# Kernel optimization log

Hardware: AMD Instinct MI355X
Metric: run time of the kernel (lower is better)

The kernel has to match this reference:

```python
import jax, jax.numpy as jnp
import numpy as np

V, E, H, T, B, L = 50000, 256, 256, 20, 64, 512
START, STOP = 18, 19
NEG = -10000.0


def setup_inputs() -> dict:
    key = jax.random.key(0)
    ks = jax.random.split(key, 16)
    lengths = jnp.sort(jax.random.randint(ks[0], (B,), 1, L + 1))[::-1]
    lengths = lengths.at[0].set(L)  # pack_padded requires sorted descending
    sentences = jax.random.randint(ks[1], (B, L), 0, V)
    s = lambda k, shp, sc: jax.random.normal(k, shp, jnp.float32) * sc
    trans = jax.random.normal(ks[12], (T, T), jnp.float32)
    trans = trans.at[START, :].set(NEG).at[:, STOP].set(NEG)
    return {
        "sentences": sentences,
        "lengths": lengths,
        "emb": s(ks[2], (V, E), 1.0),
        "w_ih_f": s(ks[3], (4 * H, E), 0.05),
        "w_hh_f": s(ks[4], (4 * H, H), 0.05),
        "b_ih_f": s(ks[5], (4 * H,), 0.05),
        "b_hh_f": s(ks[6], (4 * H,), 0.05),
        "w_ih_b": s(ks[7], (4 * H, E), 0.05),
        "w_hh_b": s(ks[8], (4 * H, H), 0.05),
        "b_ih_b": s(ks[9], (4 * H,), 0.05),
        "b_hh_b": s(ks[10], (4 * H,), 0.05),
        "w_out": s(ks[11], (T, 2 * H), 0.05),
        "b_out": s(ks[13], (T,), 0.05),
        "transitions": trans,
    }


def _lstm(x, mask, w_ih, w_hh, b_ih, b_hh):
    # x: [B,L,E]; mask: [B,L] bool. Masked scan == packed-sequence LSTM
    # (hidden frozen past length, outputs zero past length like pad_packed).
    h0 = jnp.zeros((x.shape[0], H), x.dtype)
    bias = b_ih + b_hh

    def step(carry, inp):
        h, c = carry
        xt, mt = inp
        g = xt @ w_ih.T + h @ w_hh.T + bias
        i, f, gg, o = jnp.split(g, 4, axis=-1)  # torch gate order i,f,g,o
        c_new = jax.nn.sigmoid(f) * c + jax.nn.sigmoid(i) * jnp.tanh(gg)
        h_new = jax.nn.sigmoid(o) * jnp.tanh(c_new)
        m = mt[:, None]
        h = jnp.where(m, h_new, h)
        c = jnp.where(m, c_new, c)
        return (h, c), jnp.where(m, h_new, 0.0)

    _, hs = jax.lax.scan(step, (h0, h0), (x.transpose(1, 0, 2), mask.T))
    return hs.transpose(1, 0, 2)  # [B,L,H]


def _emissions(sentences, lengths, emb, w_ih_f, w_hh_f, b_ih_f, b_hh_f,
               w_ih_b, w_hh_b, b_ih_b, b_hh_b, w_out, b_out):
    mask = jnp.arange(L)[None, :] < lengths[:, None]  # [B,L]
    embeds = emb[sentences]  # [B,L,E]
    out_f = _lstm(embeds, mask, w_ih_f, w_hh_f, b_ih_f, b_hh_f)
    # backward dir: reverse each sequence within its own length
    rev_idx = jnp.clip(lengths[:, None] - 1 - jnp.arange(L)[None, :], 0, L - 1)
    x_rev = jnp.take_along_axis(embeds, rev_idx[:, :, None], axis=1)
    h_rev = _lstm(x_rev, mask, w_ih_b, w_hh_b, b_ih_b, b_hh_b)
    out_b = jnp.take_along_axis(h_rev, rev_idx[:, :, None], axis=1) * mask[..., None]
    lstm_out = jnp.concatenate([out_f, out_b], axis=-1)  # [B,L,2H]
    return lstm_out @ w_out.T + b_out  # [B,L,T]


def _viterbi(scores, lengths, transitions):
    mask = jnp.arange(L)[None, :] < lengths[:, None]
    fv0 = jnp.full((B, T), NEG, scores.dtype).at[:, START].set(0.0)

    def step(fv, inp):
        sc_t, m_t = inp  # [B,T], [B]
        ntv = fv[:, None, :] + transitions[None]  # [B,T(next),T(prev)]
        best = jnp.argmax(ntv, axis=-1)
        fv_new = jnp.max(ntv, axis=-1) + sc_t
        fv = jnp.where(m_t[:, None], fv_new, fv)
        bp = jnp.where(m_t[:, None], best, STOP)
        return fv, bp

    fv, bps = jax.lax.scan(step, fv0, (scores.transpose(1, 0, 2), mask.T))
    terminal = fv + transitions[STOP][None, :]  # [B,T]
    last_best = jnp.argmax(terminal, axis=-1)  # [B]
    path_scores = jnp.take_along_axis(terminal, last_best[:, None], axis=1)[:, 0]

    # backtrace: j runs L-1..1; writes tag for position j-1 when j < length
    barange = jnp.arange(B)

    def back(cur, j):
        valid = j < lengths
        new = jnp.where(valid, bps[j, barange, cur], cur)
        return new, new

    js = jnp.arange(L - 1, 0, -1)
    _, tags_rev = jax.lax.scan(back, last_best, js)  # [L-1,B]
    tags = tags_rev[::-1].T  # [B,L-1], positions 0..L-2
    pos = jnp.arange(L)[None, :]
    paths = jnp.where(pos < (lengths - 1)[:, None],
                      jnp.pad(tags, ((0, 0), (0, 1))), 0)
    paths = paths.at[barange, lengths - 1].set(last_best)  # pad past length with 0
    return path_scores, paths


def reference(sentences, lengths, emb, w_ih_f, w_hh_f, b_ih_f, b_hh_f,
              w_ih_b, w_hh_b, b_ih_b, b_hh_b, w_out, b_out, transitions):
    scores = _emissions(sentences, lengths, emb, w_ih_f, w_hh_f, b_ih_f, b_hh_f,
                        w_ih_b, w_hh_b, b_ih_b, b_hh_b, w_out, b_out)
    path_scores, paths = _viterbi(scores, lengths, transitions)
    return path_scores, paths
```

## Files before the change

kernel.cpp:

```cpp
#include <hip/hip_runtime.h>
#include <hip/hip_bf16.h>
#include <math.h>

#define NV 50000
#define NE 256
#define NH 256
#define NT 20
#define NB 64
#define NL 512
#define TAG_START 18
#define TAG_STOP 19
#define NEGV -10000.0f

typedef unsigned short ushortT;
typedef __attribute__((ext_vector_type(4))) float f32x4;
typedef __attribute__((ext_vector_type(8))) short short8;

#define PINV(x) asm volatile("" : "+v"(x))

__device__ __forceinline__ float sigf_slow(float x) { return 1.0f / (1.0f + expf(-x)); }
__device__ __forceinline__ float fsig(float x) { return 1.0f / (1.0f + __expf(-x)); }
__device__ __forceinline__ float ftanh(float x) { return 1.0f - 2.0f / (1.0f + __expf(2.0f * x)); }
__device__ __forceinline__ ushortT f2bf(float f) {
    unsigned int u = __float_as_uint(f);
    u += 0x7fffu + ((u >> 16) & 1u);
    return (ushortT)(u >> 16);
}
__device__ __forceinline__ float bf2f(unsigned int bits16) {
    return __uint_as_float(bits16 << 16);
}


__global__ __launch_bounds__(256) void k_cvtw(
    const float* __restrict__ whh_f, const float* __restrict__ whh_b,
    const float* __restrict__ wih_f, const float* __restrict__ wih_b,
    ushortT* __restrict__ whh16, ushortT* __restrict__ wih16)
{
    int idx = blockIdx.x * 256 + threadIdx.x;
    const float* s; ushortT* d;
    switch (blockIdx.y) {
        case 0: s = whh_f; d = whh16;            break;
        case 1: s = whh_b; d = whh16 + 262144;   break;
        case 2: s = wih_f; d = wih16;            break;
        default: s = wih_b; d = wih16 + 262144;  break;
    }
    d[idx] = f2bf(s[idx]);
}

__global__ __launch_bounds__(1024) void k_bias(
    const float* __restrict__ bih_f, const float* __restrict__ bhh_f,
    const float* __restrict__ bih_b, const float* __restrict__ bhh_b,
    float* __restrict__ biasc)
{
    int n = threadIdx.x;
    if (blockIdx.x == 0) biasc[n] = bih_f[n] + bhh_f[n];
    else                 biasc[1024 + n] = bih_b[n] + bhh_b[n];
}

__global__
__attribute__((amdgpu_flat_work_group_size(512, 512)))
__attribute__((amdgpu_waves_per_eu(2, 2)))
void k_gin_mfma(
    const int* __restrict__ sent, const int* __restrict__ lens,
    const float* __restrict__ emb, const ushortT* __restrict__ wih16,
    const float* __restrict__ biasc, float* __restrict__ gin,
    int chunk_start, int CH)
{
    const int g = blockIdx.x, tsub = blockIdx.y;
    const int dir = blockIdx.z >> 1, half = blockIdx.z & 1;
    const int gmax = lens[g * 16];
    const int tt0 = tsub * 16;
    if (chunk_start + tt0 >= gmax) return;

    const int tid = threadIdx.x;
    const int w = tid >> 6, l = tid & 63, lr = l & 15, lg = l >> 4;

    __shared__ char x_raw[16 * 512];

    const int ucol = half * 128 + w * 16 + lr;
    short8 bfr[4][8];
    float bias_l[4];
    const ushortT* wsrc = wih16 + dir * 262144;
#pragma unroll
    for (int nt = 0; nt < 4; ++nt) {
        int col = nt * 256 + ucol;
        bias_l[nt] = biasc[dir * 1024 + col];
#pragma unroll
        for (int kt = 0; kt < 8; ++kt)
            bfr[nt][kt] = *(const short8*)(wsrc + (size_t)col * 256 + kt * 32 + lg * 8);
    }
#pragma unroll
    for (int nt = 0; nt < 4; ++nt) {
        PINV(bias_l[nt]);
#pragma unroll
        for (int kt = 0; kt < 8; ++kt) PINV(bfr[nt][kt]);
    }

    const int srow = tid >> 5, sseg = tid & 31;
    const int slen = lens[g * 16 + srow];
    const int sb = (g * 16 + srow) * 512;

    for (int i = 0; i < 16; ++i) {
        int tg = chunk_start + tt0 + i;
        if (tg >= gmax) break;

        int tsrc = dir ? (slen - 1 - tg) : tg;
        if (tsrc < 0) tsrc = 0;
        if (tsrc > 511) tsrc = 511;
        int tok = sent[sb + tsrc];
        const float* es = emb + (size_t)tok * 256 + sseg * 8;
        float4 e0 = *(const float4*)es;
        float4 e1 = *(const float4*)(es + 4);
        short8 xv;
        xv[0] = (short)f2bf(e0.x); xv[1] = (short)f2bf(e0.y);
        xv[2] = (short)f2bf(e0.z); xv[3] = (short)f2bf(e0.w);
        xv[4] = (short)f2bf(e1.x); xv[5] = (short)f2bf(e1.y);
        xv[6] = (short)f2bf(e1.z); xv[7] = (short)f2bf(e1.w);
        int sa = (srow * 512 + sseg * 16) ^ ((srow & 7) << 4);
        *(short8*)&x_raw[sa] = xv;
        __syncthreads();

        short8 af[8];
#pragma unroll
        for (int kt = 0; kt < 8; ++kt) {
            int a = (lr * 512 + kt * 64 + lg * 16) ^ ((lr & 7) << 4);
            af[kt] = *(const short8*)&x_raw[a];
        }
        f32x4 acc[4];
#pragma unroll
        for (int nt = 0; nt < 4; ++nt) {
            acc[nt][0] = bias_l[nt]; acc[nt][1] = bias_l[nt];
            acc[nt][2] = bias_l[nt]; acc[nt][3] = bias_l[nt];
        }
#pragma unroll
        for (int kt = 0; kt < 8; ++kt)
#pragma unroll
            for (int nt = 0; nt < 4; ++nt)
                acc[nt] = __builtin_amdgcn_mfma_f32_16x16x32_bf16(af[kt], bfr[nt][kt], acc[nt], 0, 0, 0);

        float* ginp = gin + ((size_t)((dir * 4 + g) * CH + (tt0 + i))) * 16384;
#pragma unroll
        for (int nt = 0; nt < 4; ++nt)
            *(f32x4*)(ginp + (nt * 256 + ucol) * 16 + lg * 4) = acc[nt];
        __syncthreads();
    }
}

__global__
__attribute__((amdgpu_flat_work_group_size(512, 512)))
__attribute__((amdgpu_waves_per_eu(2, 2)))
void k_rec_mfma(
    const int* __restrict__ lens, const ushortT* __restrict__ whh16,
    const float* __restrict__ gin, ushortT* __restrict__ hout,
    ushortT* __restrict__ st_h, float* __restrict__ st_c,
    ushortT* __restrict__ hex, unsigned int* __restrict__ flags,
    int chunk_start, int CH)
{
    const int g = blockIdx.x, dir = blockIdx.y, half = blockIdx.z;
    const int gmax = lens[g * 16];
    const int nsteps = min(CH, gmax - chunk_start);
    if (nsteps <= 0) return;

    const int tid = threadIdx.x;
    const int w = tid >> 6, l = tid & 63, lr = l & 15, lg = l >> 4;

    __shared__ char h_s[2][8192];

    int lenr[4];
#pragma unroll
    for (int r = 0; r < 4; ++r) lenr[r] = lens[g * 16 + lg * 4 + r];

    const int ucol = half * 128 + w * 16 + lr;
    short8 bfr[4][8];
    {
        const ushortT* wsrc = whh16 + dir * 262144;
#pragma unroll
        for (int nt = 0; nt < 4; ++nt) {
            const ushortT* wp = wsrc + (size_t)(nt * 256 + ucol) * 256 + lg * 8;
#pragma unroll
            for (int kt = 0; kt < 8; ++kt)
                bfr[nt][kt] = *(const short8*)(wp + kt * 32);
        }
    }
#pragma unroll
    for (int nt = 0; nt < 4; ++nt)
#pragma unroll
        for (int kt = 0; kt < 8; ++kt) PINV(bfr[nt][kt]);

    float c[4];
    if (chunk_start == 0) {
#pragma unroll
        for (int r = 0; r < 4; ++r) c[r] = 0.0f;
        for (int i = tid; i < 2048; i += 512) ((int*)h_s[0])[i] = 0;
    } else {
        const float* cs = st_c + ((size_t)((dir * 4 + g) * 2 + half)) * 2048 + tid * 4;
#pragma unroll
        for (int r = 0; r < 4; ++r) c[r] = cs[r];
        const int* hs = (const int*)st_h + (dir * 4 + g) * 2048;
        for (int i = tid; i < 2048; i += 512) ((int*)h_s[0])[i] = hs[i];
    }
    __syncthreads();

    unsigned int* exu = (unsigned int*)(hex + (dir * 4 + g) * 8192);
    unsigned int* flagMe = flags + (dir * 4 + g) * 2 + half;
    unsigned int* flagPeer = flags + (dir * 4 + g) * 2 + (half ^ 1);

    int own_lds[2], own_gid[2], peer_lds[2], peer_gid[2];
#pragma unroll
    for (int s2 = 0; s2 < 2; ++s2) {
        int i = tid * 2 + s2;
        int row = i >> 6, j = i & 63;
        int mu = half * 128 + j * 2;
        own_lds[s2] = (row * 512 + mu * 2) ^ ((row & 7) << 4);
        own_gid[s2] = row * 128 + half * 64 + j;
        int pu = (half ^ 1) * 128 + j * 2;
        peer_lds[s2] = (row * 512 + pu * 2) ^ ((row & 7) << 4);
        peer_gid[s2] = row * 128 + (half ^ 1) * 64 + j;
    }

    const float* ginp = gin + ((size_t)((dir * 4 + g) * CH)) * 16384;
    int p = 0;
    for (int tt = 0; tt < nsteps; ++tt) {
        const int t_glob = chunk_start + tt;

        f32x4 gv[4];
#pragma unroll
        for (int nt = 0; nt < 4; ++nt)
            gv[nt] = *(const f32x4*)(ginp + (size_t)tt * 16384 + (nt * 256 + ucol) * 16 + lg * 4);

        const char* hb = h_s[p];
        f32x4 acc[4];
#pragma unroll
        for (int nt = 0; nt < 4; ++nt) { acc[nt][0] = 0.f; acc[nt][1] = 0.f; acc[nt][2] = 0.f; acc[nt][3] = 0.f; }
#pragma unroll
        for (int kt = 0; kt < 8; ++kt) {
            int a_ = (lr * 512 + kt * 64 + lg * 16) ^ ((lr & 7) << 4);
            short8 af = *(const short8*)&hb[a_];
#pragma unroll
            for (int nt = 0; nt < 4; ++nt)
                acc[nt] = __builtin_amdgcn_mfma_f32_16x16x32_bf16(af, bfr[nt][kt], acc[nt], 0, 0, 0);
        }

        char* hw = h_s[p ^ 1];
#pragma unroll
        for (int r = 0; r < 4; ++r) {
            float i_ = acc[0][r] + gv[0][r];
            float f_ = acc[1][r] + gv[1][r];
            float g_ = acc[2][r] + gv[2][r];
            float o_ = acc[3][r] + gv[3][r];
            float cn = fsig(f_) * c[r] + fsig(i_) * ftanh(g_);
            float hn = fsig(o_) * ftanh(cn);
            c[r] = cn;
            ushortT hb16 = f2bf(hn);
            int row = lg * 4 + r;
            int a_ = (row * 512 + ucol * 2) ^ ((row & 7) << 4);
            *(ushortT*)&hw[a_] = hb16;
            if (t_glob < lenr[r]) {
                int tp = dir ? (lenr[r] - 1 - t_glob) : t_glob;
                hout[((size_t)((g * 16 + row) * 512 + tp)) * 512 + dir * 256 + ucol] = hb16;
            }
        }
        __syncthreads();

        unsigned int* exs = exu + ((t_glob + 1) & 1) * 2048;
#pragma unroll
        for (int s2 = 0; s2 < 2; ++s2) {
            unsigned int v = *(const unsigned int*)&hw[own_lds[s2]];
            __hip_atomic_store(&exs[own_gid[s2]], v, __ATOMIC_RELAXED, __HIP_MEMORY_SCOPE_AGENT);
        }
        __syncthreads();

        if (tid == 0) {
            __hip_atomic_store(flagMe, (unsigned int)(t_glob + 1), __ATOMIC_RELEASE, __HIP_MEMORY_SCOPE_AGENT);
            int guard = 0;
            while (__hip_atomic_load(flagPeer, __ATOMIC_RELAXED, __HIP_MEMORY_SCOPE_AGENT) < (unsigned int)(t_glob + 1)
                   && ++guard < (1 << 16)) {}
        }
        __syncthreads();

#pragma unroll
        for (int s2 = 0; s2 < 2; ++s2) {
            unsigned int v = __hip_atomic_load(&exs[peer_gid[s2]], __ATOMIC_RELAXED, __HIP_MEMORY_SCOPE_AGENT);
            *(unsigned int*)&hw[peer_lds[s2]] = v;
        }
        __syncthreads();
        p ^= 1;
    }

    float* cs = st_c + ((size_t)((dir * 4 + g) * 2 + half)) * 2048 + tid * 4;
#pragma unroll
    for (int r = 0; r < 4; ++r) cs[r] = c[r];
    if (half == 0) {
        int* hs = (int*)st_h + (dir * 4 + g) * 2048;
        for (int i = tid; i < 2048; i += 512) hs[i] = ((int*)h_s[p])[i];
    }
}

__global__ __launch_bounds__(256) void k_scores_bf(
    const int* __restrict__ lens, const ushortT* __restrict__ hout,
    const float* __restrict__ w_out, const float* __restrict__ b_out,
    float* __restrict__ scores)
{
    const int b = blockIdx.y;
    const int t0 = blockIdx.x * 32;
    const int len = lens[b];
    if (t0 >= len) return;

    __shared__ float w_s[20 * 513];
    __shared__ float row_s[512];
    __shared__ float part_s[20][9];
    __shared__ float bo_s[20];

    const int tid = threadIdx.x;
    for (int e = tid; e < 20 * 512; e += 256) w_s[(e >> 9) * 513 + (e & 511)] = w_out[e];
    if (tid < 20) bo_s[tid] = b_out[tid];
    __syncthreads();

    const int tend = min(t0 + 32, len);
    const int tag = tid >> 3, sl = tid & 7;
    for (int t = t0; t < tend; ++t) {
        const ushortT* hr = hout + ((size_t)(b * 512 + t)) * 512;
        unsigned int v = ((const unsigned int*)hr)[tid];
        row_s[tid * 2] = bf2f(v & 0xffffu);
        row_s[tid * 2 + 1] = bf2f(v >> 16);
        __syncthreads();
        if (tid < 160) {
            float s = 0.0f;
#pragma unroll 8
            for (int j = 0; j < 64; ++j) {
                int k = sl + (((j + tag) & 63) << 3);
                s = fmaf(w_s[tag * 513 + k], row_s[k], s);
            }
            part_s[tag][sl] = s;
        }
        __syncthreads();
        if (tid < 20) {
            float s = bo_s[tid];
#pragma unroll
            for (int j = 0; j < 8; ++j) s += part_s[tid][j];
            scores[((size_t)(b * 512 + t)) * 20 + tid] = s;
        }
        __syncthreads();
    }
}

__global__ __launch_bounds__(64) void k_viterbi_s(
    const int* __restrict__ lens, const float* __restrict__ scores,
    const float* __restrict__ trans, float* __restrict__ out)
{
    const int b = blockIdx.x;
    const int lane = threadIdx.x;
    const int len = lens[b];

    __shared__ float tr_s[20][21];
    __shared__ float fv_s[20];
    __shared__ float term_s[20];
    __shared__ unsigned char bp_s[512][20];
    __shared__ unsigned char path_s[512];

    for (int e = lane; e < 400; e += 64) tr_s[e / 20][e % 20] = trans[e];
    if (lane < 20) fv_s[lane] = (lane == TAG_START) ? 0.0f : NEGV;
    __syncthreads();

    const float* sc = scores + ((size_t)(b << 9)) * 20;
    for (int t = 0; t < len; ++t) {
        float m = 0.0f; int arg = 0;
        if (lane < 20) {
            m = fv_s[0] + tr_s[lane][0]; arg = 0;
#pragma unroll
            for (int k = 1; k < 20; ++k) {
                float v = fv_s[k] + tr_s[lane][k];
                if (v > m) { m = v; arg = k; }
            }
            m += sc[t * 20 + lane];
        }
        __syncthreads();
        if (lane < 20) { fv_s[lane] = m; bp_s[t][lane] = (unsigned char)arg; }
        __syncthreads();
    }

    if (lane < 20) term_s[lane] = fv_s[lane] + tr_s[TAG_STOP][lane];
    __syncthreads();

    if (lane == 0) {
        float m = term_s[0]; int arg = 0;
        for (int k = 1; k < 20; ++k) if (term_s[k] > m) { m = term_s[k]; arg = k; }
        out[b] = m;
        int cur = arg;
        path_s[len - 1] = (unsigned char)cur;
        for (int j = len - 1; j >= 1; --j) {
            cur = bp_s[j][cur];
            path_s[j - 1] = (unsigned char)cur;
        }
    }
    __syncthreads();

    float* po = out + NB + ((size_t)b << 9);
    for (int p = lane; p < NL; p += 64) po[p] = (p < len) ? (float)path_s[p] : 0.0f;
}

__global__ __launch_bounds__(256) void k_transpose_fb(
    const float* __restrict__ whh_f, const float* __restrict__ whh_b,
    const float* __restrict__ wih_f, const float* __restrict__ wih_b,
    float* __restrict__ thh_f, float* __restrict__ thh_b,
    float* __restrict__ tih_f, float* __restrict__ tih_b)
{
    int e = blockIdx.x * 256 + threadIdx.x;
    const float* wm; float* wt;
    switch (blockIdx.y) {
        case 0: wm = whh_f; wt = thh_f; break;
        case 1: wm = whh_b; wt = thh_b; break;
        case 2: wm = wih_f; wt = tih_f; break;
        default: wm = wih_b; wt = tih_b; break;
    }
    int n = e >> 8, k = e & 255;
    wt[k * 1024 + n] = wm[e];
}

__global__ __launch_bounds__(1024) void k_rec_fb(
    const int* __restrict__ sent, const int* __restrict__ lens,
    const float* __restrict__ emb,
    const float* __restrict__ thh_f, const float* __restrict__ thh_b,
    const float* __restrict__ tih_f, const float* __restrict__ tih_b,
    const float* __restrict__ b_ih_f, const float* __restrict__ b_hh_f,
    const float* __restrict__ b_ih_b, const float* __restrict__ b_hh_b,
    const float* __restrict__ w_out,
    float* __restrict__ sc_f, float* __restrict__ sc_b)
{
    const int b = blockIdx.x, dir = blockIdx.y;
    const int len = lens[b];
    const int n = threadIdx.x;
    const float* Whh = dir ? thh_b : thh_f;
    const float* Wih = dir ? tih_b : tih_f;
    const float* bi = dir ? b_ih_b : b_ih_f;
    const float* bh = dir ? b_hh_b : b_hh_f;
    float* scout = dir ? sc_b : sc_f;

    __shared__ float x_s[256];
    __shared__ float h_s[256];
    __shared__ float g_s[1024];
    __shared__ float bias_s[1024];
    __shared__ float wout_s[20 * 257];
    __shared__ float part_s[20][8];

    bias_s[n] = bi[n] + bh[n];
    for (int e = n; e < 20 * 256; e += 1024)
        wout_s[(e >> 8) * 257 + (e & 255)] = w_out[(e >> 8) * 512 + dir * 256 + (e & 255)];
    if (n < 256) h_s[n] = 0.0f;
    float c = 0.0f;
    __syncthreads();

    const int sbase = b << 9;
    for (int t = 0; t < len; ++t) {
        if (n < 256) {
            int ti = dir ? (len - 1 - t) : t;
            int tok = sent[sbase + ti];
            x_s[n] = emb[(size_t)tok * NE + n];
        }
        __syncthreads();
        float acc = bias_s[n];
        const float* wi = Wih + n;
        const float* wh = Whh + n;
#pragma unroll 8
        for (int k = 0; k < 256; ++k) {
            acc = fmaf(wh[(size_t)(k << 10)], h_s[k], acc);
            acc = fmaf(wi[(size_t)(k << 10)], x_s[k], acc);
        }
        g_s[n] = acc;
        __syncthreads();
        if (n < 256) {
            float ig = g_s[n], fg = g_s[n + 256], gg = g_s[n + 512], og = g_s[n + 768];
            float cn = sigf_slow(fg) * c + sigf_slow(ig) * tanhf(gg);
            float hn = sigf_slow(og) * tanhf(cn);
            c = cn; h_s[n] = hn;
        }
        __syncthreads();
        if (n < 160) {
            const int tag = n >> 3, sl = n & 7;
            const float* wrow = wout_s + tag * 257;
            float s = 0.0f;
#pragma unroll 8
            for (int j = 0; j < 32; ++j) { int k = sl + (j << 3); s = fmaf(wrow[k], h_s[k], s); }
            part_s[tag][sl] = s;
        }
        __syncthreads();
        if (n < 20) {
            float s = part_s[n][0];
#pragma unroll
            for (int j = 1; j < 8; ++j) s += part_s[n][j];
            int tp = dir ? (len - 1 - t) : t;
            scout[(size_t)(sbase + tp) * 20 + n] = s;
        }
    }
}

__global__ __launch_bounds__(64) void k_viterbi_fb(
    const int* __restrict__ lens,
    const float* __restrict__ sc_f, const float* __restrict__ sc_b,
    const float* __restrict__ b_out, const float* __restrict__ trans,
    float* __restrict__ out)
{
    const int b = blockIdx.x;
    const int lane = threadIdx.x;
    const int len = lens[b];

    __shared__ float tr_s[20][21];
    __shared__ float fv_s[20];
    __shared__ float term_s[20];
    __shared__ float bo_s[20];
    __shared__ unsigned char bp_s[512][20];
    __shared__ unsigned char path_s[512];

    for (int e = lane; e < 400; e += 64) tr_s[e / 20][e % 20] = trans[e];
    if (lane < 20) { fv_s[lane] = (lane == TAG_START) ? 0.0f : NEGV; bo_s[lane] = b_out[lane]; }
    __syncthreads();

    const size_t sb = (size_t)(b << 9) * 20;
    for (int t = 0; t < len; ++t) {
        float m = 0.0f; int arg = 0;
        if (lane < 20) {
            m = fv_s[0] + tr_s[lane][0]; arg = 0;
#pragma unroll
            for (int k = 1; k < 20; ++k) {
                float v = fv_s[k] + tr_s[lane][k];
                if (v > m) { m = v; arg = k; }
            }
            m += sc_f[sb + t * 20 + lane] + sc_b[sb + t * 20 + lane] + bo_s[lane];
        }
        __syncthreads();
        if (lane < 20) { fv_s[lane] = m; bp_s[t][lane] = (unsigned char)arg; }
        __syncthreads();
    }
    if (lane < 20) term_s[lane] = fv_s[lane] + tr_s[TAG_STOP][lane];
    __syncthreads();
    if (lane == 0) {
        float m = term_s[0]; int arg = 0;
        for (int k = 1; k < 20; ++k) if (term_s[k] > m) { m = term_s[k]; arg = k; }
        out[b] = m;
        int cur = arg;
        path_s[len - 1] = (unsigned char)cur;
        for (int j = len - 1; j >= 1; --j) { cur = bp_s[j][cur]; path_s[j - 1] = (unsigned char)cur; }
    }
    __syncthreads();
    float* po = out + NB + ((size_t)b << 9);
    for (int p = lane; p < NL; p += 64) po[p] = (p < len) ? (float)path_s[p] : 0.0f;
}

extern "C" void kernel_launch(void* const* d_in, const int* in_sizes, int n_in,
                              void* d_out, int out_size, void* d_ws, size_t ws_size,
                              hipStream_t stream)
{
    const int*   sent   = (const int*)d_in[0];
    const int*   lens   = (const int*)d_in[1];
    const float* emb    = (const float*)d_in[2];
    const float* w_ih_f = (const float*)d_in[3];
    const float* w_hh_f = (const float*)d_in[4];
    const float* b_ih_f = (const float*)d_in[5];
    const float* b_hh_f = (const float*)d_in[6];
    const float* w_ih_b = (const float*)d_in[7];
    const float* w_hh_b = (const float*)d_in[8];
    const float* b_ih_b = (const float*)d_in[9];
    const float* b_hh_b = (const float*)d_in[10];
    const float* w_out  = (const float*)d_in[11];
    const float* b_out  = (const float*)d_in[12];
    const float* trans  = (const float*)d_in[13];
    float* out = (float*)d_out;

    char* w = (char*)d_ws;
    const size_t base = 38612992;
    int CH = 0;
    const int chs[6] = {512, 256, 192, 128, 64, 32};
    for (int i = 0; i < 6; ++i)
        if (base + (size_t)chs[i] * 524288 <= ws_size) { CH = chs[i]; break; }

    if (CH) {
        ushortT* whh16 = (ushortT*)(w);
        ushortT* wih16 = (ushortT*)(w + 1048576);
        float*   biasc = (float*)(w + 2097152);
        ushortT* st_h  = (ushortT*)(w + 2105344);
        float*   st_c  = (float*)(w + 2170880);
        ushortT* hex   = (ushortT*)(w + 2301952);
        unsigned int* flags = (unsigned int*)(w + 2433024);
        float*   scores= (float*)(w + 2437120);
        ushortT* hout  = (ushortT*)(w + 5058560);
        float*   gin   = (float*)(w + base);

        hipMemsetAsync(flags, 0, 4096, stream);
        k_cvtw<<<dim3(1024, 4), 256, 0, stream>>>(w_hh_f, w_hh_b, w_ih_f, w_ih_b, whh16, wih16);
        k_bias<<<2, 1024, 0, stream>>>(b_ih_f, b_hh_f, b_ih_b, b_hh_b, biasc);

        for (int cs = 0; cs < NL; cs += CH) {
            k_gin_mfma<<<dim3(4, CH / 16, 4), 512, 0, stream>>>(
                sent, lens, emb, wih16, biasc, gin, cs, CH);
            k_rec_mfma<<<dim3(4, 2, 2), 512, 0, stream>>>(
                lens, whh16, gin, hout, st_h, st_c, hex, flags, cs, CH);
        }
        k_scores_bf<<<dim3(16, 64), 256, 0, stream>>>(lens, hout, w_out, b_out, scores);
        k_viterbi_s<<<64, 64, 0, stream>>>(lens, scores, trans, out);
    } else {
        float* ws2   = (float*)d_ws;
        float* thh_f = ws2;
        float* thh_b = thh_f + 262144;
        float* tih_f = thh_b + 262144;
        float* tih_b = tih_f + 262144;
        float* sc_f  = tih_b + 262144;
        float* sc_b  = sc_f + (size_t)NB * NL * NT;

        k_transpose_fb<<<dim3(1024, 4), 256, 0, stream>>>(
            w_hh_f, w_hh_b, w_ih_f, w_ih_b, thh_f, thh_b, tih_f, tih_b);
        k_rec_fb<<<dim3(NB, 2), 1024, 0, stream>>>(
            sent, lens, emb, thh_f, thh_b, tih_f, tih_b,
            b_ih_f, b_hh_f, b_ih_b, b_hh_b, w_out, sc_f, sc_b);
        k_viterbi_fb<<<NB, 64, 0, stream>>>(lens, sc_f, sc_b, b_out, trans, out);
    }
}
```

Measured before the change: 2.230 ms.

## Merge split recurrence blocks into one block per direction-group, dropping cross-block exchange

The LSTM recurrence used two cooperating workgroups per (direction, batch group). They swapped hidden-state halves through global memory with atomic flags and a spin-wait at every timestep. Now a single 512-thread workgroup computes all 256 hidden units. The W_hh slice is spread across three places: half pinned in AGPRs via inline asm, a quarter in about 128KB of LDS, and a quarter re-streamed from global memory each step. The accumulators are seeded with the precomputed input gates, and the next step's gate inputs are prefetched so only an LDS barrier is needed per step. This trades the per-step global handshake for twice the MFMA work per block, heavy LDS use, and extra per-step global weight traffic.

```diff
diff --git a/kernel.cpp b/kernel.cpp
--- a/kernel.cpp
+++ b/kernel.cpp
@@ -29,6 +29,43 @@
 __device__ __forceinline__ float bf2f(unsigned int bits16) {
     return __uint_as_float(bits16 << 16);
 }
+
+#define WRW(A0,A1,A2,A3,PTR) do {                                   \
+    int4 _u = *(const int4*)(PTR);                                  \
+    asm volatile("v_accvgpr_write_b32 a" #A0 ", %0\n\t"             \
+                 "v_accvgpr_write_b32 a" #A1 ", %1\n\t"             \
+                 "v_accvgpr_write_b32 a" #A2 ", %2\n\t"             \
+                 "v_accvgpr_write_b32 a" #A3 ", %3"                 \
+                 :: "v"(_u.x), "v"(_u.y), "v"(_u.z), "v"(_u.w)      \
+                 : "a" #A0, "a" #A1, "a" #A2, "a" #A3);             \
+} while (0)
+
+#define ACLOB128 \
+ "a0","a1","a2","a3","a4","a5","a6","a7","a8","a9","a10","a11","a12","a13","a14","a15",\
+ "a16","a17","a18","a19","a20","a21","a22","a23","a24","a25","a26","a27","a28","a29","a30","a31",\
+ "a32","a33","a34","a35","a36","a37","a38","a39","a40","a41","a42","a43","a44","a45","a46","a47",\
+ "a48","a49","a50","a51","a52","a53","a54","a55","a56","a57","a58","a59","a60","a61","a62","a63",\
+ "a64","a65","a66","a67","a68","a69","a70","a71","a72","a73","a74","a75","a76","a77","a78","a79",\
+ "a80","a81","a82","a83","a84","a85","a86","a87","a88","a89","a90","a91","a92","a93","a94","a95",\
+ "a96","a97","a98","a99","a100","a101","a102","a103","a104","a105","a106","a107","a108","a109","a110","a111",\
+ "a112","a113","a114","a115","a116","a117","a118","a119","a120","a121","a122","a123","a124","a125","a126","a127"
+
+#define MFMA_KT(PRE, POST, W0a,W0b, W1a,W1b, W2a,W2b, W3a,W3b, AF, WL4, WL5, S6, S7) \
+  asm volatile(PRE                                                                    \
+    "v_mfma_f32_16x16x32_bf16 %0, %8, a[" #W0a ":" #W0b "], %0\n\t"                   \
+    "v_mfma_f32_16x16x32_bf16 %1, %8, a[" #W1a ":" #W1b "], %1\n\t"                   \
+    "v_mfma_f32_16x16x32_bf16 %2, %8, a[" #W2a ":" #W2b "], %2\n\t"                   \
+    "v_mfma_f32_16x16x32_bf16 %3, %8, a[" #W3a ":" #W3b "], %3\n\t"                   \
+    "v_mfma_f32_16x16x32_bf16 %4, %8, %9, %4\n\t"                                     \
+    "v_mfma_f32_16x16x32_bf16 %5, %8, %10, %5\n\t"                                    \
+    "v_mfma_f32_16x16x32_bf16 %6, %8, %11, %6\n\t"                                    \
+    "v_mfma_f32_16x16x32_bf16 %7, %8, %12, %7" POST                                   \
+    : "+v"(acc0), "+v"(acc1), "+v"(acc2), "+v"(acc3),                                 \
+      "+v"(acc4), "+v"(acc5), "+v"(acc6), "+v"(acc7)                                  \
+    : "v"(AF), "v"(WL4), "v"(WL5), "v"(S6), "v"(S7)                                   \
+    : ACLOB128)
+
+#define BARRIER_LGKM() asm volatile("s_waitcnt lgkmcnt(0)\n\ts_barrier" ::: "memory")
 
 
 __global__ __launch_bounds__(256) void k_cvtw(
@@ -153,147 +190,195 @@
     const int* __restrict__ lens, const ushortT* __restrict__ whh16,
     const float* __restrict__ gin, ushortT* __restrict__ hout,
     ushortT* __restrict__ st_h, float* __restrict__ st_c,
-    ushortT* __restrict__ hex, unsigned int* __restrict__ flags,
     int chunk_start, int CH)
 {
-    const int g = blockIdx.x, dir = blockIdx.y, half = blockIdx.z;
+    const int g = blockIdx.x, dir = blockIdx.y;
     const int gmax = lens[g * 16];
     const int nsteps = min(CH, gmax - chunk_start);
     if (nsteps <= 0) return;
 
     const int tid = threadIdx.x;
     const int w = tid >> 6, l = tid & 63, lr = l & 15, lg = l >> 4;
+    const int dirg = dir * 4 + g;
 
     __shared__ char h_s[2][8192];
+    __shared__ char wl_s[2][65536];
 
     int lenr[4];
 #pragma unroll
     for (int r = 0; r < 4; ++r) lenr[r] = lens[g * 16 + lg * 4 + r];
 
-    const int ucol = half * 128 + w * 16 + lr;
-    short8 bfr[4][8];
+    const ushortT* wsrc = whh16 + dir * 262144;
+
     {
-        const ushortT* wsrc = whh16 + dir * 262144;
-#pragma unroll
-        for (int nt = 0; nt < 4; ++nt) {
-            const ushortT* wp = wsrc + (size_t)(nt * 256 + ucol) * 256 + lg * 8;
-#pragma unroll
-            for (int kt = 0; kt < 8; ++kt)
-                bfr[nt][kt] = *(const short8*)(wp + kt * 32);
-        }
-    }
-#pragma unroll
-    for (int nt = 0; nt < 4; ++nt)
-#pragma unroll
-        for (int kt = 0; kt < 8; ++kt) PINV(bfr[nt][kt]);
-
-    float c[4];
+        const ushortT* q0 = wsrc + (size_t)(0   + w * 32 +  0 + lr) * 256 + lg * 8;
+        const ushortT* q1 = wsrc + (size_t)(0   + w * 32 + 16 + lr) * 256 + lg * 8;
+        const ushortT* q2 = wsrc + (size_t)(256 + w * 32 +  0 + lr) * 256 + lg * 8;
+        const ushortT* q3 = wsrc + (size_t)(256 + w * 32 + 16 + lr) * 256 + lg * 8;
+        WRW(  0,  1,  2,  3, q0 +   0); WRW(  4,  5,  6,  7, q0 +  32);
+        WRW(  8,  9, 10, 11, q0 +  64); WRW( 12, 13, 14, 15, q0 +  96);
+        WRW( 16, 17, 18, 19, q0 + 128); WRW( 20, 21, 22, 23, q0 + 160);
+        WRW( 24, 25, 26, 27, q0 + 192); WRW( 28, 29, 30, 31, q0 + 224);
+        WRW( 32, 33, 34, 35, q1 +   0); WRW( 36, 37, 38, 39, q1 +  32);
+        WRW( 40, 41, 42, 43, q1 +  64); WRW( 44, 45, 46, 47, q1 +  96);
+        WRW( 48, 49, 50, 51, q1 + 128); WRW( 52, 53, 54, 55, q1 + 160);
+        WRW( 56, 57, 58, 59, q1 + 192); WRW( 60, 61, 62, 63, q1 + 224);
+        WRW( 64, 65, 66, 67, q2 +   0); WRW( 68, 69, 70, 71, q2 +  32);
+        WRW( 72, 73, 74, 75, q2 +  64); WRW( 76, 77, 78, 79, q2 +  96);
+        WRW( 80, 81, 82, 83, q2 + 128); WRW( 84, 85, 86, 87, q2 + 160);
+        WRW( 88, 89, 90, 91, q2 + 192); WRW( 92, 93, 94, 95, q2 + 224);
+        WRW( 96, 97, 98, 99, q3 +   0); WRW(100,101,102,103, q3 +  32);
+        WRW(104,105,106,107, q3 +  64); WRW(108,109,110,111, q3 +  96);
+        WRW(112,113,114,115, q3 + 128); WRW(116,117,118,119, q3 + 160);
+        WRW(120,121,122,123, q3 + 192); WRW(124,125,126,127, q3 + 224);
+    }
+
+    for (int it = 0; it < 16; ++it) {
+        int id = tid * 16 + it;
+        int ntl = id >> 12;
+        int rem = id & 4095;
+        int cc = rem >> 5, j = rem & 31;
+        int col = 512 + ((cc >> 4) * 32) + ntl * 16 + (cc & 15);
+        int4 v = *(const int4*)(wsrc + (size_t)col * 256 + j * 8);
+        int dst = (cc * 512 + j * 16) ^ ((cc & 7) << 4);
+        *(int4*)&wl_s[ntl][dst] = v;
+    }
+
+    float c[2][4];
     if (chunk_start == 0) {
 #pragma unroll
-        for (int r = 0; r < 4; ++r) c[r] = 0.0f;
+        for (int s = 0; s < 2; ++s)
+#pragma unroll
+            for (int r = 0; r < 4; ++r) c[s][r] = 0.0f;
         for (int i = tid; i < 2048; i += 512) ((int*)h_s[0])[i] = 0;
     } else {
-        const float* cs = st_c + ((size_t)((dir * 4 + g) * 2 + half)) * 2048 + tid * 4;
-#pragma unroll
-        for (int r = 0; r < 4; ++r) c[r] = cs[r];
-        const int* hs = (const int*)st_h + (dir * 4 + g) * 2048;
+        const float* cs = st_c + ((size_t)dirg * 512 + tid) * 8;
+#pragma unroll
+        for (int s = 0; s < 2; ++s)
+#pragma unroll
+            for (int r = 0; r < 4; ++r) c[s][r] = cs[s * 4 + r];
+        const int* hs = (const int*)st_h + dirg * 2048;
         for (int i = tid; i < 2048; i += 512) ((int*)h_s[0])[i] = hs[i];
     }
     __syncthreads();
 
-    unsigned int* exu = (unsigned int*)(hex + (dir * 4 + g) * 8192);
-    unsigned int* flagMe = flags + (dir * 4 + g) * 2 + half;
-    unsigned int* flagPeer = flags + (dir * 4 + g) * 2 + (half ^ 1);
-
-    int own_lds[2], own_gid[2], peer_lds[2], peer_gid[2];
-#pragma unroll
-    for (int s2 = 0; s2 < 2; ++s2) {
-        int i = tid * 2 + s2;
-        int row = i >> 6, j = i & 63;
-        int mu = half * 128 + j * 2;
-        own_lds[s2] = (row * 512 + mu * 2) ^ ((row & 7) << 4);
-        own_gid[s2] = row * 128 + half * 64 + j;
-        int pu = (half ^ 1) * 128 + j * 2;
-        peer_lds[s2] = (row * 512 + pu * 2) ^ ((row & 7) << 4);
-        peer_gid[s2] = row * 128 + (half ^ 1) * 64 + j;
-    }
-
-    const float* ginp = gin + ((size_t)((dir * 4 + g) * CH)) * 16384;
+    const float* ginp = gin + (size_t)dirg * CH * 16384;
+    const int co0 = (0   + w * 32 +  0 + lr) * 16 + lg * 4;
+    const int co1 = (0   + w * 32 + 16 + lr) * 16 + lg * 4;
+    const int co2 = (256 + w * 32 +  0 + lr) * 16 + lg * 4;
+    const int co3 = (256 + w * 32 + 16 + lr) * 16 + lg * 4;
+    const int co4 = (512 + w * 32 +  0 + lr) * 16 + lg * 4;
+    const int co5 = (512 + w * 32 + 16 + lr) * 16 + lg * 4;
+    const int co6 = (768 + w * 32 +  0 + lr) * 16 + lg * 4;
+    const int co7 = (768 + w * 32 + 16 + lr) * 16 + lg * 4;
+    const int c128 = w * 16 + lr;
+    const int u0 = w * 32 + lr, u1 = w * 32 + 16 + lr;
+
+    const ushortT* ps6 = wsrc + (size_t)(768 + w * 32 +  0 + lr) * 256 + lg * 8;
+    const ushortT* ps7 = wsrc + (size_t)(768 + w * 32 + 16 + lr) * 256 + lg * 8;
+
+#define LDH(KT)  (*(const short8*)&hb[(lr * 512 + (KT) * 64 + lg * 16) ^ ((lr & 7) << 4)])
+#define LDW(NT,KT) (*(const short8*)&wl_s[NT][(c128 * 512 + (KT) * 64 + lg * 16) ^ ((c128 & 7) << 4)])
+
+    short8 s6A0 = *(const short8*)(ps6 +   0), s7A0 = *(const short8*)(ps7 +   0);
+    short8 s6A1 = *(const short8*)(ps6 +  32), s7A1 = *(const short8*)(ps7 +  32);
+    short8 s6B0 = *(const short8*)(ps6 +  64), s7B0 = *(const short8*)(ps7 +  64);
+    short8 s6B1 = *(const short8*)(ps6 +  96), s7B1 = *(const short8*)(ps7 +  96);
+    f32x4 gv0 = *(const f32x4*)(ginp + co0);
+    f32x4 gv1 = *(const f32x4*)(ginp + co1);
+    f32x4 gv2 = *(const f32x4*)(ginp + co2);
+    f32x4 gv3 = *(const f32x4*)(ginp + co3);
+    f32x4 gv4 = *(const f32x4*)(ginp + co4);
+    f32x4 gv5 = *(const f32x4*)(ginp + co5);
+    f32x4 gv6 = *(const f32x4*)(ginp + co6);
+    f32x4 gv7 = *(const f32x4*)(ginp + co7);
+
     int p = 0;
     for (int tt = 0; tt < nsteps; ++tt) {
         const int t_glob = chunk_start + tt;
-
-        f32x4 gv[4];
-#pragma unroll
-        for (int nt = 0; nt < 4; ++nt)
-            gv[nt] = *(const f32x4*)(ginp + (size_t)tt * 16384 + (nt * 256 + ucol) * 16 + lg * 4);
+        asm volatile("" : "+v"(ps6), "+v"(ps7));
+
+        f32x4 acc0 = gv0, acc1 = gv1, acc2 = gv2, acc3 = gv3;
+        f32x4 acc4 = gv4, acc5 = gv5, acc6 = gv6, acc7 = gv7;
 
         const char* hb = h_s[p];
-        f32x4 acc[4];
-#pragma unroll
-        for (int nt = 0; nt < 4; ++nt) { acc[nt][0] = 0.f; acc[nt][1] = 0.f; acc[nt][2] = 0.f; acc[nt][3] = 0.f; }
-#pragma unroll
-        for (int kt = 0; kt < 8; ++kt) {
-            int a_ = (lr * 512 + kt * 64 + lg * 16) ^ ((lr & 7) << 4);
-            short8 af = *(const short8*)&hb[a_];
-#pragma unroll
-            for (int nt = 0; nt < 4; ++nt)
-                acc[nt] = __builtin_amdgcn_mfma_f32_16x16x32_bf16(af, bfr[nt][kt], acc[nt], 0, 0, 0);
-        }
+        short8 af, w4, w5;
+
+        af = LDH(0); w4 = LDW(0,0); w5 = LDW(1,0);
+        MFMA_KT("s_nop 1\n\t", "",   0,  3, 32, 35, 64, 67,  96, 99, af, w4, w5, s6A0, s7A0);
+        af = LDH(1); w4 = LDW(0,1); w5 = LDW(1,1);
+        MFMA_KT("", "",              4,  7, 36, 39, 68, 71, 100,103, af, w4, w5, s6A1, s7A1);
+        s6A0 = *(const short8*)(ps6 + 128); s7A0 = *(const short8*)(ps7 + 128);
+        s6A1 = *(const short8*)(ps6 + 160); s7A1 = *(const short8*)(ps7 + 160);
+        af = LDH(2); w4 = LDW(0,2); w5 = LDW(1,2);
+        MFMA_KT("", "",              8, 11, 40, 43, 72, 75, 104,107, af, w4, w5, s6B0, s7B0);
+        af = LDH(3); w4 = LDW(0,3); w5 = LDW(1,3);
+        MFMA_KT("", "",             12, 15, 44, 47, 76, 79, 108,111, af, w4, w5, s6B1, s7B1);
+        s6B0 = *(const short8*)(ps6 + 192); s7B0 = *(const short8*)(ps7 + 192);
+        s6B1 = *(const short8*)(ps6 + 224); s7B1 = *(const short8*)(ps7 + 224);
+        af = LDH(4); w4 = LDW(0,4); w5 = LDW(1,4);
+        MFMA_KT("", "",             16, 19, 48, 51, 80, 83, 112,115, af, w4, w5, s6A0, s7A0);
+        af = LDH(5); w4 = LDW(0,5); w5 = LDW(1,5);
+        MFMA_KT("", "",             20, 23, 52, 55, 84, 87, 116,119, af, w4, w5, s6A1, s7A1);
+        af = LDH(6); w4 = LDW(0,6); w5 = LDW(1,6);
+        MFMA_KT("", "",             24, 27, 56, 59, 88, 91, 120,123, af, w4, w5, s6B0, s7B0);
+        af = LDH(7); w4 = LDW(0,7); w5 = LDW(1,7);
+        MFMA_KT("", "\n\ts_nop 7\n\ts_nop 7",
+                                    28, 31, 60, 63, 92, 95, 124,127, af, w4, w5, s6B1, s7B1);
 
         char* hw = h_s[p ^ 1];
 #pragma unroll
         for (int r = 0; r < 4; ++r) {
-            float i_ = acc[0][r] + gv[0][r];
-            float f_ = acc[1][r] + gv[1][r];
-            float g_ = acc[2][r] + gv[2][r];
-            float o_ = acc[3][r] + gv[3][r];
-            float cn = fsig(f_) * c[r] + fsig(i_) * ftanh(g_);
-            float hn = fsig(o_) * ftanh(cn);
-            c[r] = cn;
+            float cn = fsig(acc2[r]) * c[0][r] + fsig(acc0[r]) * ftanh(acc4[r]);
+            float hn = fsig(acc6[r]) * ftanh(cn);
+            c[0][r] = cn;
             ushortT hb16 = f2bf(hn);
             int row = lg * 4 + r;
-            int a_ = (row * 512 + ucol * 2) ^ ((row & 7) << 4);
-            *(ushortT*)&hw[a_] = hb16;
+            *(ushortT*)&hw[(row * 512 + u0 * 2) ^ ((row & 7) << 4)] = hb16;
             if (t_glob < lenr[r]) {
                 int tp = dir ? (lenr[r] - 1 - t_glob) : t_glob;
-                hout[((size_t)((g * 16 + row) * 512 + tp)) * 512 + dir * 256 + ucol] = hb16;
+                hout[((size_t)((g * 16 + row) * 512 + tp)) * 512 + dir * 256 + u0] = hb16;
             }
         }
-        __syncthreads();
-
-        unsigned int* exs = exu + ((t_glob + 1) & 1) * 2048;
-#pragma unroll
-        for (int s2 = 0; s2 < 2; ++s2) {
-            unsigned int v = *(const unsigned int*)&hw[own_lds[s2]];
-            __hip_atomic_store(&exs[own_gid[s2]], v, __ATOMIC_RELAXED, __HIP_MEMORY_SCOPE_AGENT);
-        }
-        __syncthreads();
-
-        if (tid == 0) {
-            __hip_atomic_store(flagMe, (unsigned int)(t_glob + 1), __ATOMIC_RELEASE, __HIP_MEMORY_SCOPE_AGENT);
-            int guard = 0;
-            while (__hip_atomic_load(flagPeer, __ATOMIC_RELAXED, __HIP_MEMORY_SCOPE_AGENT) < (unsigned int)(t_glob + 1)
-                   && ++guard < (1 << 16)) {}
-        }
-        __syncthreads();
-
-#pragma unroll
-        for (int s2 = 0; s2 < 2; ++s2) {
-            unsigned int v = __hip_atomic_load(&exs[peer_gid[s2]], __ATOMIC_RELAXED, __HIP_MEMORY_SCOPE_AGENT);
-            *(unsigned int*)&hw[peer_lds[s2]] = v;
-        }
-        __syncthreads();
+#pragma unroll
+        for (int r = 0; r < 4; ++r) {
+            float cn = fsig(acc3[r]) * c[1][r] + fsig(acc1[r]) * ftanh(acc5[r]);
+            float hn = fsig(acc7[r]) * ftanh(cn);
+            c[1][r] = cn;
+            ushortT hb16 = f2bf(hn);
+            int row = lg * 4 + r;
+            *(ushortT*)&hw[(row * 512 + u1 * 2) ^ ((row & 7) << 4)] = hb16;
+            if (t_glob < lenr[r]) {
+                int tp = dir ? (lenr[r] - 1 - t_glob) : t_glob;
+                hout[((size_t)((g * 16 + row) * 512 + tp)) * 512 + dir * 256 + u1] = hb16;
+            }
+        }
+
+        s6A0 = *(const short8*)(ps6 +   0); s7A0 = *(const short8*)(ps7 +   0);
+        s6A1 = *(const short8*)(ps6 +  32); s7A1 = *(const short8*)(ps7 +  32);
+        s6B0 = *(const short8*)(ps6 +  64); s7B0 = *(const short8*)(ps7 +  64);
+        s6B1 = *(const short8*)(ps6 +  96); s7B1 = *(const short8*)(ps7 +  96);
+        {
+            int ttn = (tt + 1 < nsteps) ? (tt + 1) : tt;
+            const float* gp = ginp + (size_t)ttn * 16384;
+            gv0 = *(const f32x4*)(gp + co0); gv1 = *(const f32x4*)(gp + co1);
+            gv2 = *(const f32x4*)(gp + co2); gv3 = *(const f32x4*)(gp + co3);
+            gv4 = *(const f32x4*)(gp + co4); gv5 = *(const f32x4*)(gp + co5);
+            gv6 = *(const f32x4*)(gp + co6); gv7 = *(const f32x4*)(gp + co7);
+        }
+        BARRIER_LGKM();
         p ^= 1;
     }
-
-    float* cs = st_c + ((size_t)((dir * 4 + g) * 2 + half)) * 2048 + tid * 4;
-#pragma unroll
-    for (int r = 0; r < 4; ++r) cs[r] = c[r];
-    if (half == 0) {
-        int* hs = (int*)st_h + (dir * 4 + g) * 2048;
-        for (int i = tid; i < 2048; i += 512) hs[i] = ((int*)h_s[p])[i];
-    }
+#undef LDH
+#undef LDW
+
+    float* cs = st_c + ((size_t)dirg * 512 + tid) * 8;
+#pragma unroll
+    for (int s = 0; s < 2; ++s)
+#pragma unroll
+        for (int r = 0; r < 4; ++r) cs[s * 4 + r] = c[s][r];
+    int* hs = (int*)st_h + dirg * 2048;
+    for (int i = tid; i < 2048; i += 512) hs[i] = ((int*)h_s[p])[i];
 }
 
 __global__ __launch_bounds__(256) void k_scores_bf(
@@ -579,21 +664,18 @@
         float*   biasc = (float*)(w + 2097152);
         ushortT* st_h  = (ushortT*)(w + 2105344);
         float*   st_c  = (float*)(w + 2170880);
-        ushortT* hex   = (ushortT*)(w + 2301952);
-        unsigned int* flags = (unsigned int*)(w + 2433024);
         float*   scores= (float*)(w + 2437120);
         ushortT* hout  = (ushortT*)(w + 5058560);
         float*   gin   = (float*)(w + base);
 
-        hipMemsetAsync(flags, 0, 4096, stream);
         k_cvtw<<<dim3(1024, 4), 256, 0, stream>>>(w_hh_f, w_hh_b, w_ih_f, w_ih_b, whh16, wih16);
         k_bias<<<2, 1024, 0, stream>>>(b_ih_f, b_hh_f, b_ih_b, b_hh_b, biasc);
 
         for (int cs = 0; cs < NL; cs += CH) {
             k_gin_mfma<<<dim3(4, CH / 16, 4), 512, 0, stream>>>(
                 sent, lens, emb, wih16, biasc, gin, cs, CH);
-            k_rec_mfma<<<dim3(4, 2, 2), 512, 0, stream>>>(
-                lens, whh16, gin, hout, st_h, st_c, hex, flags, cs, CH);
+            k_rec_mfma<<<dim3(4, 2), 512, 0, stream>>>(
+                lens, whh16, gin, hout, st_h, st_c, cs, CH);
         }
         k_scores_bf<<<dim3(16, 64), 256, 0, stream>>>(lens, hout, w_out, b_out, scores);
         k_viterbi_s<<<64, 64, 0, stream>>>(lens, scores, trans, out);
```

After: 3.933 ms. 76.4% more time.

## Publish h directly from registers and spin on peer flag in all threads

Applied to the files above, without the earlier changes.

Each thread now writes its freshly computed bf16 h values straight to the global exchange buffer, packed two rows per word, instead of going through LDS and a separate republish pass. This removes two block-wide barriers per timestep in the latency-bound recurrent loop. Every thread now polls the peer flag itself rather than thread 0 polling and then signalling with a barrier, and the peer data is unpacked into LDS. The register-pinning asm on the weight fragments is also dropped, which may change register allocation. Having all threads poll adds memory traffic, and ordering now relies on the barrier before thread 0's release store.

```diff
diff --git a/kernel.cpp b/kernel.cpp
--- a/kernel.cpp
+++ b/kernel.cpp
@@ -153,7 +153,7 @@
     const int* __restrict__ lens, const ushortT* __restrict__ whh16,
     const float* __restrict__ gin, ushortT* __restrict__ hout,
     ushortT* __restrict__ st_h, float* __restrict__ st_c,
-    ushortT* __restrict__ hex, unsigned int* __restrict__ flags,
+    unsigned int* __restrict__ hexu, unsigned int* __restrict__ flags,
     int chunk_start, int CH)
 {
     const int g = blockIdx.x, dir = blockIdx.y, half = blockIdx.z;
@@ -163,6 +163,7 @@
 
     const int tid = threadIdx.x;
     const int w = tid >> 6, l = tid & 63, lr = l & 15, lg = l >> 4;
+    const int dirg = dir * 4 + g;
 
     __shared__ char h_s[2][8192];
 
@@ -182,10 +183,6 @@
                 bfr[nt][kt] = *(const short8*)(wp + kt * 32);
         }
     }
-#pragma unroll
-    for (int nt = 0; nt < 4; ++nt)
-#pragma unroll
-        for (int kt = 0; kt < 8; ++kt) PINV(bfr[nt][kt]);
 
     float c[4];
     if (chunk_start == 0) {
@@ -193,32 +190,34 @@
         for (int r = 0; r < 4; ++r) c[r] = 0.0f;
         for (int i = tid; i < 2048; i += 512) ((int*)h_s[0])[i] = 0;
     } else {
-        const float* cs = st_c + ((size_t)((dir * 4 + g) * 2 + half)) * 2048 + tid * 4;
+        const float* cs = st_c + ((size_t)(dirg * 2 + half)) * 2048 + tid * 4;
 #pragma unroll
         for (int r = 0; r < 4; ++r) c[r] = cs[r];
-        const int* hs = (const int*)st_h + (dir * 4 + g) * 2048;
+        const int* hs = (const int*)st_h + dirg * 2048;
         for (int i = tid; i < 2048; i += 512) ((int*)h_s[0])[i] = hs[i];
     }
     __syncthreads();
 
-    unsigned int* exu = (unsigned int*)(hex + (dir * 4 + g) * 8192);
-    unsigned int* flagMe = flags + (dir * 4 + g) * 2 + half;
-    unsigned int* flagPeer = flags + (dir * 4 + g) * 2 + (half ^ 1);
-
-    int own_lds[2], own_gid[2], peer_lds[2], peer_gid[2];
+    unsigned int* exu = hexu + dirg * 4096;
+    unsigned int* flagMe = flags + dirg * 2 + half;
+    unsigned int* flagPeer = flags + dirg * 2 + (half ^ 1);
+
+    const int pub_base = ucol * 8 + lg * 2;
+
+    int pf_uidx[2], pf_lds0[2], pf_lds1[2];
 #pragma unroll
     for (int s2 = 0; s2 < 2; ++s2) {
         int i = tid * 2 + s2;
-        int row = i >> 6, j = i & 63;
-        int mu = half * 128 + j * 2;
-        own_lds[s2] = (row * 512 + mu * 2) ^ ((row & 7) << 4);
-        own_gid[s2] = row * 128 + half * 64 + j;
-        int pu = (half ^ 1) * 128 + j * 2;
-        peer_lds[s2] = (row * 512 + pu * 2) ^ ((row & 7) << 4);
-        peer_gid[s2] = row * 128 + (half ^ 1) * 64 + j;
-    }
-
-    const float* ginp = gin + ((size_t)((dir * 4 + g) * CH)) * 16384;
+        int pcol = ((half ^ 1) << 7) + (i >> 3);
+        int sub = i & 7;
+        pf_uidx[s2] = pcol * 8 + sub;
+        int r0 = (sub >> 1) * 4 + (sub & 1) * 2;
+        pf_lds0[s2] = (r0 * 512 + pcol * 2) ^ ((r0 & 7) << 4);
+        int r1 = r0 + 1;
+        pf_lds1[s2] = (r1 * 512 + pcol * 2) ^ ((r1 & 7) << 4);
+    }
+
+    const float* ginp = gin + (size_t)dirg * CH * 16384;
     int p = 0;
     for (int tt = 0; tt < nsteps; ++tt) {
         const int t_glob = chunk_start + tt;
@@ -242,6 +241,8 @@
         }
 
         char* hw = h_s[p ^ 1];
+        unsigned int* exs = exu + ((t_glob + 1) & 1) * 2048;
+        ushortT hh[4];
 #pragma unroll
         for (int r = 0; r < 4; ++r) {
             float i_ = acc[0][r] + gv[0][r];
@@ -251,47 +252,50 @@
             float cn = fsig(f_) * c[r] + fsig(i_) * ftanh(g_);
             float hn = fsig(o_) * ftanh(cn);
             c[r] = cn;
-            ushortT hb16 = f2bf(hn);
+            hh[r] = f2bf(hn);
             int row = lg * 4 + r;
-            int a_ = (row * 512 + ucol * 2) ^ ((row & 7) << 4);
-            *(ushortT*)&hw[a_] = hb16;
+            *(ushortT*)&hw[(row * 512 + ucol * 2) ^ ((row & 7) << 4)] = hh[r];
+        }
+        unsigned int v01 = (unsigned int)hh[0] | ((unsigned int)hh[1] << 16);
+        unsigned int v23 = (unsigned int)hh[2] | ((unsigned int)hh[3] << 16);
+        __hip_atomic_store(&exs[pub_base + 0], v01, __ATOMIC_RELAXED, __HIP_MEMORY_SCOPE_AGENT);
+        __hip_atomic_store(&exs[pub_base + 1], v23, __ATOMIC_RELAXED, __HIP_MEMORY_SCOPE_AGENT);
+#pragma unroll
+        for (int r = 0; r < 4; ++r) {
             if (t_glob < lenr[r]) {
+                int row = lg * 4 + r;
                 int tp = dir ? (lenr[r] - 1 - t_glob) : t_glob;
-                hout[((size_t)((g * 16 + row) * 512 + tp)) * 512 + dir * 256 + ucol] = hb16;
+                hout[((size_t)((g * 16 + row) * 512 + tp)) * 512 + dir * 256 + ucol] = hh[r];
             }
         }
-        __syncthreads();
-
-        unsigned int* exs = exu + ((t_glob + 1) & 1) * 2048;
+
+        __syncthreads();
+
+        if (tid == 0)
+            __hip_atomic_store(flagMe, (unsigned int)(t_glob + 1), __ATOMIC_RELEASE, __HIP_MEMORY_SCOPE_AGENT);
+
+        {
+            unsigned int tgt = (unsigned int)(t_glob + 1);
+            int guard = 0;
+            while (__hip_atomic_load(flagPeer, __ATOMIC_RELAXED, __HIP_MEMORY_SCOPE_AGENT) < tgt
+                   && ++guard < (1 << 16)) {}
+        }
+
 #pragma unroll
         for (int s2 = 0; s2 < 2; ++s2) {
-            unsigned int v = *(const unsigned int*)&hw[own_lds[s2]];
-            __hip_atomic_store(&exs[own_gid[s2]], v, __ATOMIC_RELAXED, __HIP_MEMORY_SCOPE_AGENT);
-        }
-        __syncthreads();
-
-        if (tid == 0) {
-            __hip_atomic_store(flagMe, (unsigned int)(t_glob + 1), __ATOMIC_RELEASE, __HIP_MEMORY_SCOPE_AGENT);
-            int guard = 0;
-            while (__hip_atomic_load(flagPeer, __ATOMIC_RELAXED, __HIP_MEMORY_SCOPE_AGENT) < (unsigned int)(t_glob + 1)
-                   && ++guard < (1 << 16)) {}
-        }
-        __syncthreads();
-
-#pragma unroll
-        for (int s2 = 0; s2 < 2; ++s2) {
-            unsigned int v = __hip_atomic_load(&exs[peer_gid[s2]], __ATOMIC_RELAXED, __HIP_MEMORY_SCOPE_AGENT);
-            *(unsigned int*)&hw[peer_lds[s2]] = v;
+            unsigned int v = __hip_atomic_load(&exs[pf_uidx[s2]], __ATOMIC_RELAXED, __HIP_MEMORY_SCOPE_AGENT);
+            *(ushortT*)&hw[pf_lds0[s2]] = (ushortT)(v & 0xffffu);
+            *(ushortT*)&hw[pf_lds1[s2]] = (ushortT)(v >> 16);
         }
         __syncthreads();
         p ^= 1;
     }
 
-    float* cs = st_c + ((size_t)((dir * 4 + g) * 2 + half)) * 2048 + tid * 4;
+    float* cs = st_c + ((size_t)(dirg * 2 + half)) * 2048 + tid * 4;
 #pragma unroll
     for (int r = 0; r < 4; ++r) cs[r] = c[r];
     if (half == 0) {
-        int* hs = (int*)st_h + (dir * 4 + g) * 2048;
+        int* hs = (int*)st_h + dirg * 2048;
         for (int i = tid; i < 2048; i += 512) hs[i] = ((int*)h_s[p])[i];
     }
 }
@@ -579,7 +583,7 @@
         float*   biasc = (float*)(w + 2097152);
         ushortT* st_h  = (ushortT*)(w + 2105344);
         float*   st_c  = (float*)(w + 2170880);
-        ushortT* hex   = (ushortT*)(w + 2301952);
+        unsigned int* hexu = (unsigned int*)(w + 2301952);
         unsigned int* flags = (unsigned int*)(w + 2433024);
         float*   scores= (float*)(w + 2437120);
         ushortT* hout  = (ushortT*)(w + 5058560);
@@ -593,7 +597,7 @@
             k_gin_mfma<<<dim3(4, CH / 16, 4), 512, 0, stream>>>(
                 sent, lens, emb, wih16, biasc, gin, cs, CH);
             k_rec_mfma<<<dim3(4, 2, 2), 512, 0, stream>>>(
-                lens, whh16, gin, hout, st_h, st_c, hex, flags, cs, CH);
+                lens, whh16, gin, hout, st_h, st_c, hexu, flags, cs, CH);
         }
         k_scores_bf<<<dim3(16, 64), 256, 0, stream>>>(lens, hout, w_out, b_out, scores);
         k_viterbi_s<<<64, 64, 0, stream>>>(lens, scores, trans, out);
```

New measurement: 2.400 ms. 7.6% more time.
